# Kernel optimization log

Hardware: AMD Instinct MI355X
Metric: run time of the kernel (lower is better)

Reference implementation:

```python
import jax, jax.numpy as jnp
import numpy as np

R = 1.1
SCALE = 100.0
BUMP_STEPS = 32
NUM_THETAS = 32
NUM_FEATURES = 128
N_NODES = 200000
NUM_GRAPHS = 128


def setup_inputs() -> dict:
    key = jax.random.key(0)
    k1, k2, k3 = jax.random.split(key, 3)
    x = jax.random.normal(k1, (N_NODES, NUM_FEATURES), dtype=jnp.float32)
    batch = jnp.sort(jax.random.randint(k2, (N_NODES,), 0, NUM_GRAPHS, dtype=jnp.int64))
    v = jax.random.uniform(k3, (NUM_THETAS, NUM_FEATURES), dtype=jnp.float32) - 0.5
    return {"x": x, "batch": batch, "num_graphs": NUM_GRAPHS, "v": v}


def reference(x, batch, num_graphs, v):
    # nh: node heights along each direction theta -> [N, T]
    nh = x @ v.T
    # linspace over filtration values -> [S]
    lin = jnp.linspace(-R, R, BUMP_STEPS, dtype=nh.dtype)
    # bump: sigmoid difference; second point is the constant pad value R
    # ecc: [N, S, T]  (node-major so segment_sum reduces the leading axis)
    ecc = (jax.nn.sigmoid(SCALE * (lin[None, :, None] - nh[:, None, :]))
           - jax.nn.sigmoid(SCALE * (lin - R))[None, :, None])
    # scatter-add per graph label -> [ng, S, T] == index_add over dim1 then movedim(0,1)
    ect = jax.ops.segment_sum(ecc, batch, num_segments=num_graphs)
    return ect
```

## Files before the change

kernel.cpp:

```cpp
#include <hip/hip_runtime.h>
#include <math.h>

#define N_NODES 200000
#define NF 128
#define NT 32
#define NS 32
#define NG 128
#define ATILE 64
#define ABLOCKS 3125
#define VSTRIDE 136
#define HPAD 33

typedef short bf16x8 __attribute__((ext_vector_type(8)));
typedef float floatx4 __attribute__((ext_vector_type(4)));

__device__ __forceinline__ float rcp_fast(float x) { return __builtin_amdgcn_rcpf(x); }

__device__ __forceinline__ void split_bf16(float f, unsigned short& h, unsigned short& l) {
    unsigned u  = __float_as_uint(f);
    unsigned r  = u + 0x7FFFu + ((u >> 16) & 1u);
    unsigned hb = r & 0xFFFF0000u;
    h = (unsigned short)(hb >> 16);
    float rem = f - __uint_as_float(hb);
    unsigned u2 = __float_as_uint(rem);
    unsigned r2 = u2 + 0x7FFFu + ((u2 >> 16) & 1u);
    l = (unsigned short)(r2 >> 16);
}

__device__ __forceinline__ void split8(float4 a, float4 b, bf16x8& h8, bf16x8& l8) {
    unsigned short h[8], l[8];
    split_bf16(a.x, h[0], l[0]); split_bf16(a.y, h[1], l[1]);
    split_bf16(a.z, h[2], l[2]); split_bf16(a.w, h[3], l[3]);
    split_bf16(b.x, h[4], l[4]); split_bf16(b.y, h[5], l[5]);
    split_bf16(b.z, h[6], l[6]); split_bf16(b.w, h[7], l[7]);
    h8 = (bf16x8){(short)h[0],(short)h[1],(short)h[2],(short)h[3],
                  (short)h[4],(short)h[5],(short)h[6],(short)h[7]};
    l8 = (bf16x8){(short)l[0],(short)l[1],(short)l[2],(short)l[3],
                  (short)l[4],(short)l[5],(short)l[6],(short)l[7]};
}

__global__ __launch_bounds__(256, 4)
void ect_fused(const float* __restrict__ x,
               const int* __restrict__ batch,
               const float* __restrict__ v,
               float* __restrict__ out)
{
    __shared__ unsigned short vh[NT * VSTRIDE];
    __shared__ unsigned short vl[NT * VSTRIDE];
    __shared__ int      batch_lds[ATILE];
    __shared__ unsigned hist[NT * HPAD];
    __shared__ float    corr[NT * HPAD];
    __shared__ float    cnt_lds;

    const int tid  = threadIdx.x;
    const int blk  = blockIdx.x;
    const int w    = tid >> 6;
    const int lane = tid & 63;
    const int mrow = lane & 15;
    const int quad = lane >> 4;

    #pragma unroll
    for (int j = 0; j < 4; ++j) {
        int idx4 = j * 256 + tid;
        int row  = idx4 >> 5;
        int f4   = idx4 & 31;
        float4 val = *(const float4*)&v[(size_t)row * NF + f4 * 4];
        unsigned short h0,h1,h2,h3,l0,l1,l2,l3;
        split_bf16(val.x, h0, l0); split_bf16(val.y, h1, l1);
        split_bf16(val.z, h2, l2); split_bf16(val.w, h3, l3);
        uint2 hh, ll;
        hh.x = (unsigned)h0 | ((unsigned)h1 << 16); hh.y = (unsigned)h2 | ((unsigned)h3 << 16);
        ll.x = (unsigned)l0 | ((unsigned)l1 << 16); ll.y = (unsigned)l2 | ((unsigned)l3 << 16);
        *(uint2*)&vh[row * VSTRIDE + f4 * 4] = hh;
        *(uint2*)&vl[row * VSTRIDE + f4 * 4] = ll;
    }
    if (tid < ATILE) batch_lds[tid] = batch[blk * ATILE + tid];

    const size_t arow = (size_t)blk * ATILE + w * 16 + mrow;
    const float* __restrict__ xrow = x + arow * NF + quad * 8;

    floatx4 acc0 = {0.f, 0.f, 0.f, 0.f};
    floatx4 acc1 = {0.f, 0.f, 0.f, 0.f};

    bf16x8 ah[4], al[4];
    #pragma unroll
    for (int slice = 0; slice < 4; ++slice) {
        float4 a0 = *(const float4*)&xrow[slice * 32];
        float4 a1 = *(const float4*)&xrow[slice * 32 + 4];
        split8(a0, a1, ah[slice], al[slice]);
    }
    __syncthreads();

    const int b0base = mrow * VSTRIDE + quad * 8;
    const int b1base = (16 + mrow) * VSTRIDE + quad * 8;
    #pragma unroll
    for (int slice = 0; slice < 4; ++slice) {
        bf16x8 bh0 = *(bf16x8*)&vh[b0base + slice * 32];
        bf16x8 bl0 = *(bf16x8*)&vl[b0base + slice * 32];
        bf16x8 bh1 = *(bf16x8*)&vh[b1base + slice * 32];
        bf16x8 bl1 = *(bf16x8*)&vl[b1base + slice * 32];
        acc0 = __builtin_amdgcn_mfma_f32_16x16x32_bf16(ah[slice], bh0, acc0, 0, 0, 0);
        acc0 = __builtin_amdgcn_mfma_f32_16x16x32_bf16(ah[slice], bl0, acc0, 0, 0, 0);
        acc0 = __builtin_amdgcn_mfma_f32_16x16x32_bf16(al[slice], bh0, acc0, 0, 0, 0);
        acc1 = __builtin_amdgcn_mfma_f32_16x16x32_bf16(ah[slice], bh1, acc1, 0, 0, 0);
        acc1 = __builtin_amdgcn_mfma_f32_16x16x32_bf16(ah[slice], bl1, acc1, 0, 0, 0);
        acc1 = __builtin_amdgcn_mfma_f32_16x16x32_bf16(al[slice], bh1, acc1, 0, 0, 0);
    }

    const float inv_dlin = 14.090909090909092f;
    const float Lw       = 10.23848093f;
    const float dlin     = 2.2f / 31.0f;
    const float L        = 144.26950408889634f;

    const int g_first = batch_lds[0];
    const int g_last  = batch_lds[ATILE - 1];

    const int ft = tid & 31;
    const int sb = tid >> 5;

    for (int gp = g_first; gp <= g_last; ++gp) {
        for (int i = tid; i < NT * HPAD; i += 256) { hist[i] = 0u; corr[i] = 0.0f; }
        __syncthreads();

        #pragma unroll
        for (int reg = 0; reg < 4; ++reg) {
            int n = w * 16 + quad * 4 + reg;
            if (batch_lds[n] == gp) {
                #pragma unroll
                for (int half = 0; half < 2; ++half) {
                    int   t = half ? (16 + mrow) : mrow;
                    float h = half ? acc1[reg] : acc0[reg];
                    float z = fmaf(h, inv_dlin, 15.5f);
                    int s_up = (int)ceilf(z);
                    s_up = min(max(s_up, 0), 32);
                    atomicAdd(&hist[t * HPAD + s_up], 1u);
                    int s0 = (int)ceilf(z - 1.45f);
                    #pragma unroll
                    for (int i2 = 0; i2 < 3; ++i2) {
                        int s = s0 + i2;
                        float e   = __builtin_amdgcn_exp2f(Lw * (z - (float)s));
                        float sig = rcp_fast(1.0f + e);
                        float stp = (s >= s_up) ? 1.0f : 0.0f;
                        if (s >= 0 && s <= 31) atomicAdd(&corr[t * HPAD + s], sig - stp);
                    }
                }
            }
        }
        __syncthreads();

        if (tid < ATILE) {
            unsigned long long m = __ballot(batch_lds[tid] == gp);
            if (tid == 0) cnt_lds = (float)__popcll(m);
        }
        {
            const int grp = tid >> 5;
            const int s   = tid & 31;
            for (int row = grp; row < NT; row += 8) {
                float val = (float)hist[row * HPAD + s];
                #pragma unroll
                for (int d = 1; d < 32; d <<= 1) {
                    float nbr = __shfl_up(val, d, 32);
                    if (s >= d) val += nbr;
                }
                corr[row * HPAD + s] += val;
            }
        }
        __syncthreads();

        #pragma unroll
        for (int k = 0; k < 4; ++k) {
            int s = sb + 8 * k;
            float lin_s = -1.1f + (float)s * dlin;
            float cs  = rcp_fast(1.0f + __builtin_amdgcn_exp2f(L * (1.1f - lin_s)));
            float val = corr[ft * HPAD + s] - cnt_lds * cs;
            atomicAdd(&out[(size_t)gp * (NS * NT) + s * NT + ft], val);
        }
        if (gp < g_last) __syncthreads();
    }
}

extern "C" void kernel_launch(void* const* d_in, const int* in_sizes, int n_in,
                              void* d_out, int out_size, void* d_ws, size_t ws_size,
                              hipStream_t stream) {
    const float* x     = (const float*)d_in[0];
    const int*   batch = (const int*)d_in[1];
    const float* v     = (const float*)d_in[3];
    float*       out   = (float*)d_out;

    hipMemsetAsync(d_out, 0, (size_t)out_size * sizeof(float), stream);
    ect_fused<<<dim3(ABLOCKS), dim3(256), 0, stream>>>(x, batch, v, out);
}
```

Before: 169.8 us.

## Compact transitional nodes into LDS queue and use difference-form corrections with single prefix scan

Replaces the separate integer histogram and per-node sigmoid corrections with one difference array. Nodes that fall fully below the range become plain counts, and only nodes near the range boundary are compacted via ballot/mbcnt into a per-wave LDS queue (reusing the vh buffer). The queue is then processed with the whole block, using one exp2 plus scaled products for the neighbouring sigmoids. The change also hoists the constant per-step sigmoid term out of the graph loop, drops the hist array and raises launch bounds occupancy. Reusing vh as the queue needs an extra barrier, and it swaps 33-bin integer atomics for float atomics with the corrections written as differences.

```diff
diff --git a/kernel.cpp b/kernel.cpp
--- a/kernel.cpp
+++ b/kernel.cpp
@@ -1,11 +1,9 @@
 #include <hip/hip_runtime.h>
 #include <math.h>
 
-#define N_NODES 200000
 #define NF 128
 #define NT 32
 #define NS 32
-#define NG 128
 #define ATILE 64
 #define ABLOCKS 3125
 #define VSTRIDE 136
@@ -39,18 +37,18 @@
                   (short)l[4],(short)l[5],(short)l[6],(short)l[7]};
 }
 
-__global__ __launch_bounds__(256, 4)
+__global__ __launch_bounds__(256, 7)
 void ect_fused(const float* __restrict__ x,
                const int* __restrict__ batch,
                const float* __restrict__ v,
                float* __restrict__ out)
 {
-    __shared__ unsigned short vh[NT * VSTRIDE];
-    __shared__ unsigned short vl[NT * VSTRIDE];
-    __shared__ int      batch_lds[ATILE];
-    __shared__ unsigned hist[NT * HPAD];
-    __shared__ float    corr[NT * HPAD];
-    __shared__ float    cnt_lds;
+    __shared__ __align__(16) unsigned short vh[NT * VSTRIDE];
+    __shared__ __align__(16) unsigned short vl[NT * VSTRIDE];
+    __shared__ int   batch_lds[ATILE];
+    __shared__ float corr[NT * HPAD];
+    __shared__ float cnt_lds;
+    __shared__ int   qcnt[4];
 
     const int tid  = threadIdx.x;
     const int blk  = blockIdx.x;
@@ -106,63 +104,109 @@
         acc1 = __builtin_amdgcn_mfma_f32_16x16x32_bf16(ah[slice], bl1, acc1, 0, 0, 0);
         acc1 = __builtin_amdgcn_mfma_f32_16x16x32_bf16(al[slice], bh1, acc1, 0, 0, 0);
     }
+    __syncthreads();
+
+    float* qf = (float*)vh;
 
     const float inv_dlin = 14.090909090909092f;
     const float Lw       = 10.23848093f;
     const float dlin     = 2.2f / 31.0f;
     const float L        = 144.26950408889634f;
+    const float C1       = 8.2777115e-04f;
 
     const int g_first = batch_lds[0];
     const int g_last  = batch_lds[ATILE - 1];
 
     const int ft = tid & 31;
     const int sb = tid >> 5;
+    float csk[4];
+    #pragma unroll
+    for (int k = 0; k < 4; ++k) {
+        int s = sb + 8 * k;
+        float lin_s = -1.1f + (float)s * dlin;
+        csk[k] = rcp_fast(1.0f + __builtin_amdgcn_exp2f(L * (1.1f - lin_s)));
+    }
+
+    const float cH0 = 31.5f + 64.0f * (float)mrow;
+    const float cH1 = cH0 + 1024.0f;
+    const float lo0 = cH0 - 16.95f, hi0 = cH0 + 16.95f;
+    const float lo1 = cH1 - 16.95f, hi1 = cH1 + 16.95f;
 
     for (int gp = g_first; gp <= g_last; ++gp) {
-        for (int i = tid; i < NT * HPAD; i += 256) { hist[i] = 0u; corr[i] = 0.0f; }
-        __syncthreads();
-
+        for (int i = tid; i < NT * HPAD; i += 256) corr[i] = 0.0f;
+        if (tid < ATILE) {
+            unsigned long long m2 = __ballot(batch_lds[tid] == gp);
+            if (tid == 0) cnt_lds = (float)__popcll(m2);
+        }
+        int wbase = w * 512;
+        int c0 = 0, c1 = 0;
         #pragma unroll
         for (int reg = 0; reg < 4; ++reg) {
-            int n = w * 16 + quad * 4 + reg;
-            if (batch_lds[n] == gp) {
-                #pragma unroll
-                for (int half = 0; half < 2; ++half) {
-                    int   t = half ? (16 + mrow) : mrow;
-                    float h = half ? acc1[reg] : acc0[reg];
-                    float z = fmaf(h, inv_dlin, 15.5f);
-                    int s_up = (int)ceilf(z);
-                    s_up = min(max(s_up, 0), 32);
-                    atomicAdd(&hist[t * HPAD + s_up], 1u);
-                    int s0 = (int)ceilf(z - 1.45f);
-                    #pragma unroll
-                    for (int i2 = 0; i2 < 3; ++i2) {
-                        int s = s0 + i2;
-                        float e   = __builtin_amdgcn_exp2f(Lw * (z - (float)s));
-                        float sig = rcp_fast(1.0f + e);
-                        float stp = (s >= s_up) ? 1.0f : 0.0f;
-                        if (s >= 0 && s <= 31) atomicAdd(&corr[t * HPAD + s], sig - stp);
-                    }
-                }
-            }
-        }
+            bool ok = (batch_lds[w * 16 + quad * 4 + reg] == gp);
+            {
+                float zt = fmaf(acc0[reg], inv_dlin, cH0);
+                bool full = ok && (zt > lo0) && (zt < hi0);
+                unsigned long long m = __ballot(full);
+                int pos = __builtin_amdgcn_mbcnt_hi((unsigned)(m >> 32),
+                          __builtin_amdgcn_mbcnt_lo((unsigned)m, 0));
+                if (full) qf[wbase + pos] = zt;
+                wbase += __popcll(m);
+                c0 += (ok && (zt <= lo0)) ? 1 : 0;
+            }
+            {
+                float zt = fmaf(acc1[reg], inv_dlin, cH1);
+                bool full = ok && (zt > lo1) && (zt < hi1);
+                unsigned long long m = __ballot(full);
+                int pos = __builtin_amdgcn_mbcnt_hi((unsigned)(m >> 32),
+                          __builtin_amdgcn_mbcnt_lo((unsigned)m, 0));
+                if (full) qf[wbase + pos] = zt;
+                wbase += __popcll(m);
+                c1 += (ok && (zt <= lo1)) ? 1 : 0;
+            }
+        }
+        if (lane == 0) qcnt[w] = wbase - w * 512;
         __syncthreads();
 
-        if (tid < ATILE) {
-            unsigned long long m = __ballot(batch_lds[tid] == gp);
-            if (tid == 0) cnt_lds = (float)__popcll(m);
-        }
+        if (c0) atomicAdd(&corr[mrow * HPAD], (float)c0);
+        if (c1) atomicAdd(&corr[(16 + mrow) * HPAD], (float)c1);
+        for (int seg = 0; seg < 4; ++seg) {
+            const int ne = qcnt[seg];
+            for (int i = tid; i < ne; i += 256) {
+                float zt  = qf[seg * 512 + i];
+                float tf  = floorf(zt * 0.015625f);
+                float z   = fmaf(tf, -64.0f, zt) - 16.0f;
+                int   b   = (int)tf * HPAD;
+                float s0f = ceilf(z - 1.45f);
+                int   s0  = (int)s0f;
+                float e0  = __builtin_amdgcn_exp2f(Lw * (z - s0f));
+                float e1  = e0 * C1;
+                float e2  = e1 * C1;
+                float f0  = rcp_fast(1.0f + e0);
+                float f1  = rcp_fast(1.0f + e1);
+                float f2  = rcp_fast(1.0f + e2);
+                int sA = max(s0, 0);
+                atomicAdd(&corr[b + sA], f0);
+                int sB = max(s0 + 1, 0);
+                if (sB < 32) atomicAdd(&corr[b + sB], f1 - f0);
+                int sC = max(s0 + 2, 0);
+                if (sC < 32) atomicAdd(&corr[b + sC], f2 - f1);
+                int sD = s0 + 3;
+                if (sD < 32) atomicAdd(&corr[b + sD], 1.0f - f2);
+            }
+        }
+        __syncthreads();
+
         {
             const int grp = tid >> 5;
-            const int s   = tid & 31;
+            const int sc  = tid & 31;
             for (int row = grp; row < NT; row += 8) {
-                float val = (float)hist[row * HPAD + s];
+                float val = corr[row * HPAD + sc];
                 #pragma unroll
                 for (int d = 1; d < 32; d <<= 1) {
                     float nbr = __shfl_up(val, d, 32);
-                    if (s >= d) val += nbr;
+                    if (sc >= d) val += nbr;
                 }
-                corr[row * HPAD + s] += val;
+                corr[row * HPAD + sc] = val;
             }
         }
         __syncthreads();
@@ -170,9 +214,7 @@
         #pragma unroll
         for (int k = 0; k < 4; ++k) {
             int s = sb + 8 * k;
-            float lin_s = -1.1f + (float)s * dlin;
-            float cs  = rcp_fast(1.0f + __builtin_amdgcn_exp2f(L * (1.1f - lin_s)));
-            float val = corr[ft * HPAD + s] - cnt_lds * cs;
+            float val = corr[ft * HPAD + s] - cnt_lds * csk[k];
             atomicAdd(&out[(size_t)gp * (NS * NT) + s * NT + ft], val);
         }
         if (gp < g_last) __syncthreads();
```

New measurement: 183.6 us. 1.08x slower.
